# Performance work log

Measured on AMD Instinct MI355X. Metric: run time of the kernel, lower is better.

## Reference

```python
import jax, jax.numpy as jnp
import numpy as np

D_MODEL = 1024
N_HEADS = 16
HEAD_DIM = D_MODEL // N_HEADS
D_FF = 4096
LN_EPS = 1e-5


def setup_inputs() -> dict:
    key = jax.random.key(0)
    ks = jax.random.split(key, 13)
    s = lambda fan_in: 1.0 / np.sqrt(fan_in)
    return {
        "x": jax.random.normal(ks[0], (2, 2048, D_MODEL), dtype=jnp.float32),
        "w_qkv": jax.random.uniform(ks[1], (D_MODEL, 3 * D_MODEL), jnp.float32, -s(D_MODEL), s(D_MODEL)),
        "b_qkv": jax.random.uniform(ks[2], (3 * D_MODEL,), jnp.float32, -s(D_MODEL), s(D_MODEL)),
        "w_out": jax.random.uniform(ks[3], (D_MODEL, D_MODEL), jnp.float32, -s(D_MODEL), s(D_MODEL)),
        "b_out": jax.random.uniform(ks[4], (D_MODEL,), jnp.float32, -s(D_MODEL), s(D_MODEL)),
        "w_ff1": jax.random.uniform(ks[5], (D_MODEL, D_FF), jnp.float32, -s(D_MODEL), s(D_MODEL)),
        "b_ff1": jax.random.uniform(ks[6], (D_FF,), jnp.float32, -s(D_MODEL), s(D_MODEL)),
        "w_ff2": jax.random.uniform(ks[7], (D_FF, D_MODEL), jnp.float32, -s(D_FF), s(D_FF)),
        "b_ff2": jax.random.uniform(ks[8], (D_MODEL,), jnp.float32, -s(D_FF), s(D_FF)),
        "ln1_g": jnp.ones((D_MODEL,), jnp.float32),
        "ln1_b": jnp.zeros((D_MODEL,), jnp.float32),
        "ln2_g": jnp.ones((D_MODEL,), jnp.float32),
        "ln2_b": jnp.zeros((D_MODEL,), jnp.float32),
    }


def _layer_norm(x, g, b):
    mu = jnp.mean(x, axis=-1, keepdims=True)
    var = jnp.mean(jnp.square(x - mu), axis=-1, keepdims=True)
    return (x - mu) * jax.lax.rsqrt(var + LN_EPS) * g + b


def reference(x, w_qkv, b_qkv, w_out, b_out, w_ff1, b_ff1, w_ff2, b_ff2,
              ln1_g, ln1_b, ln2_g, ln2_b):
    B, S, D = x.shape
    scale = HEAD_DIM ** -0.5
    qkv = x @ w_qkv + b_qkv                                   # [B,S,3D]
    qkv = qkv.reshape(B, S, 3, N_HEADS, HEAD_DIM)
    q, k, v = (qkv[:, :, 0], qkv[:, :, 1], qkv[:, :, 2])      # [B,S,H,Dh]
    attn = jnp.einsum("bqhd,bkhd->bhqk", q, k) * scale        # [B,H,S,S]
    attn = jax.nn.softmax(attn, axis=-1)
    o = jnp.einsum("bhqk,bkhd->bqhd", attn, v).reshape(B, S, D)
    o = o @ w_out + b_out
    x = _layer_norm(x + o, ln1_g, ln1_b)
    # FFN: Linear -> exact GELU -> Linear (dropout = 0)
    h = jax.nn.gelu(x @ w_ff1 + b_ff1, approximate=False)
    ff = h @ w_ff2 + b_ff2
    x = _layer_norm(x + ff, ln2_g, ln2_b)
    return x
```

## Files before the change

### kernel.cpp

```cpp
#include <hip/hip_runtime.h>
#include <hip/hip_bf16.h>
#include <cstdint>
#include <cstddef>

using bf16 = __hip_bfloat16;
typedef __attribute__((ext_vector_type(8))) short bf16x8;
typedef __attribute__((ext_vector_type(4))) float f32x4;

#define TOKENS 4096
#define DMODEL 1024
#define DFF    4096
#define SEQ    2048
#define NHEAD  16
#define HDIM   64
#define KVBLK  64
#define NT     (SEQ / KVBLK)
#define QSCALE 0.1803368801111f

__device__ __forceinline__ void async16(const void* g, void* l) {
  __builtin_amdgcn_global_load_lds(
      (const __attribute__((address_space(1))) void*)g,
      (__attribute__((address_space(3))) void*)l, 16, 0, 0);
}

__device__ __forceinline__ f32x4 mfma16(bf16x8 a, bf16x8 b, f32x4 c) {
  return __builtin_amdgcn_mfma_f32_16x16x32_bf16(a, b, c, 0, 0, 0);
}

__device__ __forceinline__ float exp2_fast(float x) {
  float r;
  asm("v_exp_f32 %0, %1" : "=v"(r) : "v"(x));
  return r;
}

__device__ __forceinline__ float gelu_fast(float x) {
  const float z = fabsf(x) * 0.70710678118f;
  const float t = __builtin_amdgcn_rcpf(1.f + 0.3275911f * z);
  float p = 1.061405429f;
  p = p * t - 1.453152027f;
  p = p * t + 1.421413741f;
  p = p * t - 0.284496736f;
  p = p * t + 0.254829592f;
  const float e = exp2_fast(-z * z * 1.44269504089f);
  float erf = 1.f - p * t * e;
  erf = (x < 0.f) ? -erf : erf;
  return 0.5f * x * (1.f + erf);
}

__global__ __launch_bounds__(256)
void prep_k(const float* __restrict__ wqkv, const float* __restrict__ wout,
            const float* __restrict__ wff1, const float* __restrict__ wff2,
            bf16* __restrict__ dqkv, bf16* __restrict__ dout,
            bf16* __restrict__ dff1, bf16* __restrict__ dff2,
            const float* __restrict__ x, bf16* __restrict__ xb) {
  const int b = blockIdx.x, t = threadIdx.x;
  if (b >= 12288) {
    const int i = (b - 12288) * 1024 + t * 4;
    float4 v = *(const float4*)(x + i);
    bf16* d = xb + i;
    d[0] = __float2bfloat16(v.x); d[1] = __float2bfloat16(v.y);
    d[2] = __float2bfloat16(v.z); d[3] = __float2bfloat16(v.w);
    return;
  }
  const float* src; bf16* dst; int K, N, local;
  if (b < 3072)      { src = wqkv; dst = dqkv; K = 1024; N = 3072; local = b; }
  else if (b < 4096) { src = wout; dst = dout; K = 1024; N = 1024; local = b - 3072; }
  else if (b < 8192) { src = wff1; dst = dff1; K = 1024; N = 4096; local = b - 4096; }
  else               { src = wff2; dst = dff2; K = 4096; N = 1024; local = b - 8192; }
  const int nx = N >> 5;
  const int tiley = local / nx, tilex = local - tiley * nx;
  const int nt = tilex * 32, kt = tiley * 32;
  const int tx = t & 31, ty = t >> 5;
  __shared__ float tile[32][33];
  #pragma unroll
  for (int i = 0; i < 32; i += 8)
    tile[ty + i][tx] = src[(size_t)(kt + ty + i) * N + nt + tx];
  __syncthreads();
  #pragma unroll
  for (int i = 0; i < 32; i += 8)
    dst[(size_t)(nt + ty + i) * K + kt + tx] = __float2bfloat16(tile[tx][ty + i]);
}

template <int EPI, int BN>
__global__ __launch_bounds__(256, 2)
void gemm_bt(const bf16* __restrict__ A, const bf16* __restrict__ Bt,
             const float* __restrict__ bias, int M, int N, int K,
             float* __restrict__ outf, float* __restrict__ outf2,
             bf16* __restrict__ outb,
             bf16* __restrict__ Qb, bf16* __restrict__ Kb, bf16* __restrict__ Vtb) {
  constexpr int MR = (BN == 128) ? 4 : 2;
  __shared__ bf16 Al[2][128 * 32];
  __shared__ bf16 Bl[2][BN * 32];
  const int t = threadIdx.x;
  const int nwg = gridDim.x * gridDim.y;
  const int flat = blockIdx.y * gridDim.x + blockIdx.x;
  const int swz = (flat & 7) * (nwg >> 3) + (flat >> 3);
  const int bm = (swz / gridDim.x) * 128, bn = (swz % gridDim.x) * BN;
  const int kz = blockIdx.z;
  const int Ksub = K / gridDim.z;
  const int kb0 = kz * Ksub;
  const int wid = t >> 6, lane = t & 63, g = lane >> 4, r = lane & 15;
  const int wr = (BN == 128) ? (wid >> 1) * 64 : wid * 32;
  const int wc = (BN == 128) ? (wid & 1) * 64 : 0;

  const f32x4 zero = {0.f, 0.f, 0.f, 0.f};
  f32x4 acc[MR][4];
  #pragma unroll
  for (int i = 0; i < MR; i++)
    #pragma unroll
    for (int j = 0; j < 4; j++) acc[i][j] = zero;

  const int ar0 = t >> 2, ac = (t & 3) * 8;
  const int ar1 = ar0 + 64;
  const int ach0 = t * 16, ach1 = ach0 + 4096;

  const int NK = Ksub >> 5;
  #define STAGE(ktile, pb)                                                          \
    do {                                                                            \
      const int kk = kb0 + ((ktile) << 5);                                          \
      async16(A + (size_t)(bm + ar0) * K + kk + ac, (char*)Al[pb] + ach0);          \
      async16(A + (size_t)(bm + ar1) * K + kk + ac, (char*)Al[pb] + ach1);          \
      async16(Bt + (size_t)(bn + ar0) * K + kk + ac, (char*)Bl[pb] + ach0);         \
      if constexpr (BN == 128)                                                      \
        async16(Bt + (size_t)(bn + ar1) * K + kk + ac, (char*)Bl[pb] + ach1);       \
    } while (0)

  STAGE(0, 0);
  asm volatile("s_waitcnt vmcnt(0)" ::: "memory");
  __builtin_amdgcn_s_barrier();

  #pragma unroll 1
  for (int it = 0; it < NK; ++it) {
    const int cur = it & 1;
    if (it + 1 < NK) STAGE(it + 1, cur ^ 1);
    bf16x8 af[MR], bfr[4];
    #pragma unroll
    for (int mt = 0; mt < MR; mt++)
      af[mt] = *(const bf16x8*)&Al[cur][(wr + mt * 16 + r) * 32 + 8 * g];
    #pragma unroll
    for (int nt = 0; nt < 4; nt++)
      bfr[nt] = *(const bf16x8*)&Bl[cur][(wc + nt * 16 + r) * 32 + 8 * g];
    #pragma unroll
    for (int mt = 0; mt < MR; mt++)
      #pragma unroll
      for (int nt = 0; nt < 4; nt++)
        acc[mt][nt] = mfma16(af[mt], bfr[nt], acc[mt][nt]);
    __builtin_amdgcn_sched_barrier(0);
    asm volatile("s_waitcnt vmcnt(0)" ::: "memory");
    __builtin_amdgcn_s_barrier();
  }
  #undef STAGE

  float* __restrict__ pdst = kz ? outf2 : outf;
  #pragma unroll
  for (int nt = 0; nt < 4; nt++) {
    const int col = bn + wc + nt * 16 + r;
    const float bv = (EPI == 3) ? 0.f : bias[col];
    #pragma unroll
    for (int mt = 0; mt < MR; mt++) {
      #pragma unroll
      for (int j = 0; j < 4; j++) {
        const int row = bm + wr + mt * 16 + 4 * g + j;
        float v = acc[mt][nt][j] + bv;
        if constexpr (EPI == 0) {
          const int part = col >> 10, hd = col & 1023, h = hd >> 6, d = hd & 63;
          const int b_ = row >> 11, s_ = row & 2047;
          if (part == 0) {
            Qb[((size_t)(b_ * NHEAD + h) * SEQ + s_) * HDIM + d] =
                __float2bfloat16(v * QSCALE);
          } else if (part == 1) {
            Kb[((size_t)(b_ * NHEAD + h) * SEQ + s_) * HDIM + d] = __float2bfloat16(v);
          } else {
            Vtb[((size_t)(b_ * NHEAD + h) * HDIM + d) * SEQ + s_] = __float2bfloat16(v);
          }
        } else if constexpr (EPI == 3) {
          pdst[(size_t)row * N + col] = v;
        } else {
          outb[(size_t)row * N + col] = __float2bfloat16(gelu_fast(v));
        }
      }
    }
  }
}

__global__ __launch_bounds__(256, 3)
void attn_k(const bf16* __restrict__ Q, const bf16* __restrict__ Km,
            const bf16* __restrict__ Vt, bf16* __restrict__ O) {
  __shared__ bf16 Kl[2][KVBLK * 64];
  __shared__ bf16 Vl[2][KVBLK * 64];
  __shared__ bf16 P[4][32 * 64];
  const int b = blockIdx.x;
  const int bswz = (b & 7) * 64 + (b >> 3);
  const int bh = bswz >> 4, qb = bswz & 15;
  const int t = threadIdx.x, wid = t >> 6, lane = t & 63, g = lane >> 4, r = lane & 15;
  const int q0 = qb * 128 + wid * 32;
  const bf16* Qp = Q + (size_t)bh * SEQ * HDIM;
  const char* Kc = (const char*)(Km + (size_t)bh * SEQ * HDIM);
  const char* Vc = (const char*)(Vt + (size_t)bh * HDIM * SEQ);

  bf16x8 qf[2][2];
  #pragma unroll
  for (int s = 0; s < 2; s++) {
    qf[s][0] = *(const bf16x8*)&Qp[(q0 + 16 * s + r) * HDIM + 8 * g];
    qf[s][1] = *(const bf16x8*)&Qp[(q0 + 16 * s + r) * HDIM + 8 * g + 32];
  }

  const int o0 = wid * 2048 + lane * 16, o1 = o0 + 1024;
  const int cs0 = ((((o0 >> 4) & 7) ^ ((o0 >> 7) & 7)) << 4);
  const int cs1 = ((((o1 >> 4) & 7) ^ ((o1 >> 7) & 7)) << 4);
  const int kso0 = (o0 & ~127) + cs0, kso1 = (o1 & ~127) + cs1;
  const int vso0 = (o0 >> 7) * (SEQ * 2) + cs0, vso1 = (o1 >> 7) * (SEQ * 2) + cs1;

  const f32x4 zero = {0.f, 0.f, 0.f, 0.f};
  f32x4 oacc[2][4];
  #pragma unroll
  for (int s = 0; s < 2; s++)
    #pragma unroll
    for (int i = 0; i < 4; i++) oacc[s][i] = zero;
  float mrow[2] = {-1e30f, -1e30f}, lrow[2] = {0.f, 0.f};
  bf16* pl = P[wid];
  const int cA = ((g ^ (r & 7)) << 3), cB = (((g + 4) ^ (r & 7)) << 3);

  {
    char* kd = (char*)Kl[0]; char* vd = (char*)Vl[0];
    async16(Kc + kso0, kd + o0); async16(Kc + kso1, kd + o1);
    async16(Vc + vso0, vd + o0); async16(Vc + vso1, vd + o1);
  }

  #pragma unroll 1
  for (int tt = 0; tt < NT; ++tt) {
    if (tt + 1 < NT) {
      const char* ks = Kc + (tt + 1) * (KVBLK * HDIM * 2);
      const char* vs = Vc + (tt + 1) * (KVBLK * 2);
      char* kd = (char*)Kl[(tt + 1) & 1]; char* vd = (char*)Vl[(tt + 1) & 1];
      async16(ks + kso0, kd + o0); async16(ks + kso1, kd + o1);
      async16(vs + vso0, vd + o0); async16(vs + vso1, vd + o1);
      asm volatile("s_waitcnt vmcnt(4)" ::: "memory");
    } else {
      asm volatile("s_waitcnt vmcnt(0)" ::: "memory");
    }
    __builtin_amdgcn_sched_barrier(0);
    __builtin_amdgcn_s_barrier();
    __builtin_amdgcn_sched_barrier(0);

    const bf16* kbuf = Kl[tt & 1];
    const bf16* vbuf = Vl[tt & 1];

    f32x4 sacc[2][4];
    #pragma unroll
    for (int kt = 0; kt < 4; kt++) {
      const bf16* krow = kbuf + (kt * 16 + r) * 64;
      bf16x8 ka = *(const bf16x8*)&krow[cA];
      bf16x8 kb = *(const bf16x8*)&krow[cB];
      #pragma unroll
      for (int s = 0; s < 2; s++) {
        f32x4 sc = mfma16(ka, qf[s][0], zero);
        sacc[s][kt] = mfma16(kb, qf[s][1], sc);
      }
    }

    bool grow[2];
    float corr[2];
    #pragma unroll
    for (int s = 0; s < 2; s++) {
      float m0 = fmaxf(fmaxf(sacc[s][0][0], sacc[s][0][1]), fmaxf(sacc[s][0][2], sacc[s][0][3]));
      float m1 = fmaxf(fmaxf(sacc[s][1][0], sacc[s][1][1]), fmaxf(sacc[s][1][2], sacc[s][1][3]));
      float m2 = fmaxf(fmaxf(sacc[s][2][0], sacc[s][2][1]), fmaxf(sacc[s][2][2], sacc[s][2][3]));
      float m3 = fmaxf(fmaxf(sacc[s][3][0], sacc[s][3][1]), fmaxf(sacc[s][3][2], sacc[s][3][3]));
      float mx = fmaxf(fmaxf(m0, m1), fmaxf(m2, m3));
      mx = fmaxf(mx, __shfl_xor(mx, 16));
      mx = fmaxf(mx, __shfl_xor(mx, 32));
      grow[s] = !__all(mx <= mrow[s] + 8.f);
      corr[s] = 1.f;
      if (grow[s]) {
        const float mn = fmaxf(mrow[s], mx);
        corr[s] = exp2_fast(mrow[s] - mn);
        mrow[s] = mn;
      }
      float sum = 0.f;
      #pragma unroll
      for (int kt = 0; kt < 4; kt++) {
        bf16 pk[4];
        #pragma unroll
        for (int j = 0; j < 4; j++) {
          const float p = exp2_fast(sacc[s][kt][j] - mrow[s]);
          pk[j] = __float2bfloat16(p);
          sum += p;
        }
        const int pc = (((kt * 2 + (g >> 1)) ^ (r & 7)) << 4) + ((g & 1) << 3);
        *(short4*)((char*)pl + (16 * s + r) * 128 + pc) = *(const short4*)pk;
      }
      sum += __shfl_xor(sum, 16);
      sum += __shfl_xor(sum, 32);
      lrow[s] = lrow[s] * corr[s] + sum;
    }

    asm volatile("s_waitcnt lgkmcnt(0)" ::: "memory");
    __builtin_amdgcn_sched_barrier(0);
    bf16x8 pf[2][2];
    #pragma unroll
    for (int s = 0; s < 2; s++) {
      pf[s][0] = *(const bf16x8*)((const char*)pl + (16 * s + r) * 128 + (cA << 1));
      pf[s][1] = *(const bf16x8*)((const char*)pl + (16 * s + r) * 128 + (cB << 1));
    }

    #pragma unroll
    for (int s = 0; s < 2; s++) {
      if (grow[s]) {
        float cq[4];
        #pragma unroll
        for (int j = 0; j < 4; j++) cq[j] = __shfl(corr[s], 4 * g + j);
        #pragma unroll
        for (int dt = 0; dt < 4; dt++)
          #pragma unroll
          for (int j = 0; j < 4; j++) oacc[s][dt][j] *= cq[j];
      }
    }

    #pragma unroll
    for (int dt = 0; dt < 4; dt++) {
      const bf16* vrow = vbuf + (dt * 16 + r) * 64;
      bf16x8 v0 = *(const bf16x8*)&vrow[cA];
      bf16x8 v1 = *(const bf16x8*)&vrow[cB];
      #pragma unroll
      for (int s = 0; s < 2; s++) {
        oacc[s][dt] = mfma16(pf[s][0], v0, oacc[s][dt]);
        oacc[s][dt] = mfma16(pf[s][1], v1, oacc[s][dt]);
      }
    }
    __builtin_amdgcn_sched_barrier(0);
    __builtin_amdgcn_s_barrier();
  }

  const int b_ = bh >> 4, h = bh & 15;
  #pragma unroll
  for (int s = 0; s < 2; s++) {
    float lq[4];
    #pragma unroll
    for (int j = 0; j < 4; j++) lq[j] = __shfl(lrow[s], 4 * g + j);
    #pragma unroll
    for (int dt = 0; dt < 4; dt++)
      #pragma unroll
      for (int j = 0; j < 4; j++) {
        const int tok = b_ * SEQ + q0 + 16 * s + 4 * g + j;
        O[(size_t)tok * DMODEL + h * HDIM + dt * 16 + r] =
            __float2bfloat16(oacc[s][dt][j] / lq[j]);
      }
  }
}

__global__ __launch_bounds__(256)
void ln_fused_k(const float* __restrict__ p0, const float* __restrict__ p1,
                const float* __restrict__ bias2, const float* __restrict__ resid,
                const float* __restrict__ gw, const float* __restrict__ bw,
                float* __restrict__ outf, bf16* __restrict__ outb) {
  const int row = blockIdx.x, t = threadIdx.x;
  const size_t base = (size_t)row * DMODEL + t * 4;
  const float4 a = *(const float4*)(p0 + base);
  const float4 b = *(const float4*)(p1 + base);
  const float4 rr = *(const float4*)(resid + base);
  const float4 bb = *(const float4*)(bias2 + t * 4);
  float4 v;
  v.x = a.x + b.x + rr.x + bb.x;
  v.y = a.y + b.y + rr.y + bb.y;
  v.z = a.z + b.z + rr.z + bb.z;
  v.w = a.w + b.w + rr.w + bb.w;
  float s = v.x + v.y + v.z + v.w;
  float s2 = v.x * v.x + v.y * v.y + v.z * v.z + v.w * v.w;
  #pragma unroll
  for (int m = 1; m < 64; m <<= 1) { s += __shfl_xor(s, m); s2 += __shfl_xor(s2, m); }
  __shared__ float red[8];
  const int wid = t >> 6, lane = t & 63;
  if (lane == 0) { red[wid] = s; red[4 + wid] = s2; }
  __syncthreads();
  s = red[0] + red[1] + red[2] + red[3];
  s2 = red[4] + red[5] + red[6] + red[7];
  const float mu = s * (1.f / DMODEL);
  const float rstd = rsqrtf(s2 * (1.f / DMODEL) - mu * mu + 1e-5f);
  const float4 gv = *(const float4*)(gw + t * 4);
  const float4 bv = *(const float4*)(bw + t * 4);
  float o0 = (v.x - mu) * rstd * gv.x + bv.x;
  float o1 = (v.y - mu) * rstd * gv.y + bv.y;
  float o2 = (v.z - mu) * rstd * gv.z + bv.z;
  float o3 = (v.w - mu) * rstd * gv.w + bv.w;
  if (outf) {
    float4 ov = {o0, o1, o2, o3};
    *(float4*)(outf + base) = ov;
  }
  if (outb) {
    bf16* p = outb + base;
    p[0] = __float2bfloat16(o0); p[1] = __float2bfloat16(o1);
    p[2] = __float2bfloat16(o2); p[3] = __float2bfloat16(o3);
  }
}

extern "C" void kernel_launch(void* const* d_in, const int* in_sizes, int n_in,
                              void* d_out, int out_size, void* d_ws, size_t ws_size,
                              hipStream_t stream) {
  const float* x     = (const float*)d_in[0];
  const float* w_qkv = (const float*)d_in[1];
  const float* b_qkv = (const float*)d_in[2];
  const float* w_out = (const float*)d_in[3];
  const float* b_out = (const float*)d_in[4];
  const float* w_ff1 = (const float*)d_in[5];
  const float* b_ff1 = (const float*)d_in[6];
  const float* w_ff2 = (const float*)d_in[7];
  const float* b_ff2 = (const float*)d_in[8];
  const float* ln1_g = (const float*)d_in[9];
  const float* ln1_b = (const float*)d_in[10];
  const float* ln2_g = (const float*)d_in[11];
  const float* ln2_b = (const float*)d_in[12];
  float* out = (float*)d_out;

  char* base = (char*)d_ws;
  bf16* wqkvT = (bf16*)(base);
  bf16* woutT = (bf16*)(base + 6291456);
  bf16* wff1T = (bf16*)(base + 8388608);
  bf16* wff2T = (bf16*)(base + 16777216);
  bf16* Qb    = (bf16*)(base + 25165824);
  bf16* Kb    = (bf16*)(base + 33554432);
  bf16* Vtb   = (bf16*)(base + 41943040);
  bf16* xob   = (bf16*)(base + 50331648);
  bf16* hb    = (bf16*)(base + 25165824);
  float* pA0  = (float*)(base + 25165824);
  float* pA1  = (float*)(base + 58720256);
  float* pB0  = (float*)(base + 58720256);
  float* pB1  = (float*)(base);
  float* x1f  = (float*)(base + 75497472);
  bf16* x1b   = (bf16*)(base + 92274688);
  (void)in_sizes; (void)n_in; (void)out_size; (void)ws_size;

  prep_k<<<dim3(16384), 256, 0, stream>>>(w_qkv, w_out, w_ff1, w_ff2,
                                          wqkvT, woutT, wff1T, wff2T, x, xob);

  gemm_bt<0, 128><<<dim3(3072 / 128, TOKENS / 128), 256, 0, stream>>>(
      xob, wqkvT, b_qkv, TOKENS, 3072, 1024, nullptr, nullptr, nullptr, Qb, Kb, Vtb);
  attn_k<<<dim3(512), 256, 0, stream>>>(Qb, Kb, Vtb, xob);
  gemm_bt<3, 64><<<dim3(1024 / 64, TOKENS / 128, 2), 256, 0, stream>>>(
      xob, woutT, b_out, TOKENS, 1024, 1024, pA0, pA1, nullptr, nullptr, nullptr, nullptr);
  ln_fused_k<<<TOKENS, 256, 0, stream>>>(pA0, pA1, b_out, x, ln1_g, ln1_b, x1f, x1b);
  gemm_bt<2, 128><<<dim3(4096 / 128, TOKENS / 128), 256, 0, stream>>>(
      x1b, wff1T, b_ff1, TOKENS, 4096, 1024, nullptr, nullptr, hb, nullptr, nullptr, nullptr);
  gemm_bt<3, 64><<<dim3(1024 / 64, TOKENS / 128, 2), 256, 0, stream>>>(
      hb, wff2T, b_ff2, TOKENS, 1024, 4096, pB0, pB1, nullptr, nullptr, nullptr, nullptr);
  ln_fused_k<<<TOKENS, 256, 0, stream>>>(pB0, pB1, b_ff2, x1f, ln2_g, ln2_b, out, nullptr);
}
```

Before: 259.9 us.

## Double GEMM K-tile to 64 with XOR-swizzled LDS layout

Raises the GEMM K-step per LDS stage from 32 to 64, which halves the number of barrier and wait iterations and issues twice as many MFMAs between syncs. The LDS tiles are stored with an XOR swizzle of 16-byte chunks by row, so the wider 128-byte rows do not cause bank conflicts on the fragment reads. In exchange, LDS use per block doubles, which may limit how many blocks fit on a CU under launch_bounds(256,2), and register pressure rises from the doubled fragment arrays.

```diff
diff --git a/kernel.cpp b/kernel.cpp
--- a/kernel.cpp
+++ b/kernel.cpp
@@ -89,8 +89,8 @@
              bf16* __restrict__ outb,
              bf16* __restrict__ Qb, bf16* __restrict__ Kb, bf16* __restrict__ Vtb) {
   constexpr int MR = (BN == 128) ? 4 : 2;
-  __shared__ bf16 Al[2][128 * 32];
-  __shared__ bf16 Bl[2][BN * 32];
+  __shared__ bf16 Al[2][128 * 64];
+  __shared__ bf16 Bl[2][BN * 64];
   const int t = threadIdx.x;
   const int nwg = gridDim.x * gridDim.y;
   const int flat = blockIdx.y * gridDim.x + blockIdx.x;
@@ -110,19 +110,27 @@
     #pragma unroll
     for (int j = 0; j < 4; j++) acc[i][j] = zero;
 
-  const int ar0 = t >> 2, ac = (t & 3) * 8;
-  const int ar1 = ar0 + 64;
-  const int ach0 = t * 16, ach1 = ach0 + 4096;
-
-  const int NK = Ksub >> 5;
+  const int cA0 = ((g ^ (r & 7)) << 3);
+  const int cA1 = (((g + 4) ^ (r & 7)) << 3);
+
+  const int NK = Ksub >> 6;
   #define STAGE(ktile, pb)                                                          \
     do {                                                                            \
-      const int kk = kb0 + ((ktile) << 5);                                          \
-      async16(A + (size_t)(bm + ar0) * K + kk + ac, (char*)Al[pb] + ach0);          \
-      async16(A + (size_t)(bm + ar1) * K + kk + ac, (char*)Al[pb] + ach1);          \
-      async16(Bt + (size_t)(bn + ar0) * K + kk + ac, (char*)Bl[pb] + ach0);         \
-      if constexpr (BN == 128)                                                      \
-        async16(Bt + (size_t)(bn + ar1) * K + kk + ac, (char*)Bl[pb] + ach1);       \
+      const int kk = kb0 + ((ktile) << 6);                                          \
+      _Pragma("unroll")                                                             \
+      for (int i = 0; i < 4; i++) {                                                 \
+        const int c = t + 256 * i;                                                  \
+        const int rw = c >> 3;                                                      \
+        const int sc = ((c ^ rw) & 7) << 3;                                         \
+        async16(A + (size_t)(bm + rw) * K + kk + sc, (char*)Al[pb] + c * 16);       \
+      }                                                                             \
+      _Pragma("unroll")                                                             \
+      for (int i = 0; i < (BN == 128 ? 4 : 2); i++) {                               \
+        const int c = t + 256 * i;                                                  \
+        const int rw = c >> 3;                                                      \
+        const int sc = ((c ^ rw) & 7) << 3;                                         \
+        async16(Bt + (size_t)(bn + rw) * K + kk + sc, (char*)Bl[pb] + c * 16);      \
+      }                                                                             \
     } while (0)
 
   STAGE(0, 0);
@@ -133,18 +141,26 @@
   for (int it = 0; it < NK; ++it) {
     const int cur = it & 1;
     if (it + 1 < NK) STAGE(it + 1, cur ^ 1);
-    bf16x8 af[MR], bfr[4];
+    bf16x8 af[MR][2], bfr[4][2];
+    #pragma unroll
+    for (int mt = 0; mt < MR; mt++) {
+      const int rb = (wr + mt * 16 + r) * 64;
+      af[mt][0] = *(const bf16x8*)&Al[cur][rb + cA0];
+      af[mt][1] = *(const bf16x8*)&Al[cur][rb + cA1];
+    }
+    #pragma unroll
+    for (int nt = 0; nt < 4; nt++) {
+      const int rb = (wc + nt * 16 + r) * 64;
+      bfr[nt][0] = *(const bf16x8*)&Bl[cur][rb + cA0];
+      bfr[nt][1] = *(const bf16x8*)&Bl[cur][rb + cA1];
+    }
     #pragma unroll
     for (int mt = 0; mt < MR; mt++)
-      af[mt] = *(const bf16x8*)&Al[cur][(wr + mt * 16 + r) * 32 + 8 * g];
-    #pragma unroll
-    for (int nt = 0; nt < 4; nt++)
-      bfr[nt] = *(const bf16x8*)&Bl[cur][(wc + nt * 16 + r) * 32 + 8 * g];
-    #pragma unroll
-    for (int mt = 0; mt < MR; mt++)
-      #pragma unroll
-      for (int nt = 0; nt < 4; nt++)
-        acc[mt][nt] = mfma16(af[mt], bfr[nt], acc[mt][nt]);
+      #pragma unroll
+      for (int nt = 0; nt < 4; nt++) {
+        acc[mt][nt] = mfma16(af[mt][0], bfr[nt][0], acc[mt][nt]);
+        acc[mt][nt] = mfma16(af[mt][1], bfr[nt][1], acc[mt][nt]);
+      }
     __builtin_amdgcn_sched_barrier(0);
     asm volatile("s_waitcnt vmcnt(0)" ::: "memory");
     __builtin_amdgcn_s_barrier();
```

Result: slower. 280.3 us (+7.8%).
